# Optimization experiments

Measured on AMD Instinct MI355X. Metric: run time of the kernel, lower is better.

## Reference

```python
import jax, jax.numpy as jnp
import numpy as np


def setup_inputs() -> dict:
    key = jax.random.key(0)
    k1, k2, k3 = jax.random.split(key, 3)
    B, L, D = 32, 8192, 512
    q = jax.random.normal(k1, (B, D), dtype=jnp.float32)
    k = jax.random.normal(k2, (B, L, D), dtype=jnp.float32)
    v = jax.random.normal(k3, (B, L, D), dtype=jnp.float32)
    return {"q": q, "k": k, "v": v}


def reference(q, k, v):
    # q: [B, D], k: [B, L, D], v: [B, L, D]
    # scores: [B, 1, L]  (single query per batch element, no 1/sqrt(d) scaling
    # in the original module)
    scores = jnp.einsum("bd,bld->bl", q, k)[:, None, :]
    # double softmax over the key dimension, exactly as the torch module
    att_weights = jax.nn.softmax(scores, axis=-1)
    att_score = jax.nn.softmax(att_weights, axis=-1)
    # ctx: [B, D]
    ctx = jnp.einsum("bsl,bld->bsd", att_score, v)[:, 0, :]
    return (ctx, att_score)
```

## Files before the change

kernel.cpp:

```cpp
#include <hip/hip_runtime.h>
#include <hip/hip_bf16.h>
#include <stdint.h>

#define B_ 32
#define L_ 8192
#define D_ 512

__global__ __launch_bounds__(256) void k_scores(const float* __restrict__ q,
                                                const float* __restrict__ k,
                                                float* __restrict__ scores) {
    int blk  = blockIdx.x;
    int b    = blk >> 7;
    int l0   = (blk & 127) << 6;
    int wave = threadIdx.x >> 6;
    int lane = threadIdx.x & 63;

    float4 q0 = *reinterpret_cast<const float4*>(q + b * D_ + lane * 4);
    float4 q1 = *reinterpret_cast<const float4*>(q + b * D_ + 256 + lane * 4);

    const size_t kbase = (size_t)b * L_ * D_;
    for (int i = 0; i < 16; i++) {
        int l = l0 + i * 4 + wave;
        const float* kr = k + kbase + (size_t)l * D_;
        float4 a0 = *reinterpret_cast<const float4*>(kr + lane * 4);
        float4 a1 = *reinterpret_cast<const float4*>(kr + 256 + lane * 4);
        float s = a0.x * q0.x + a0.y * q0.y + a0.z * q0.z + a0.w * q0.w
                + a1.x * q1.x + a1.y * q1.y + a1.z * q1.z + a1.w * q1.w;
        #pragma unroll
        for (int off = 32; off; off >>= 1) s += __shfl_xor(s, off, 64);
        if (lane == 0) scores[b * L_ + l] = s;
    }
}

__global__ __launch_bounds__(1024) void k_softmax2(float* __restrict__ sc,
                                                   float* __restrict__ att_out) {
    int b = blockIdx.x;
    int t = threadIdx.x;
    int wid = t >> 6, lane = t & 63;
    __shared__ float red[16];

    float s[8];
    #pragma unroll
    for (int j = 0; j < 8; j++) s[j] = sc[b * L_ + t + j * 1024];

    float m = s[0];
    #pragma unroll
    for (int j = 1; j < 8; j++) m = fmaxf(m, s[j]);
    #pragma unroll
    for (int off = 32; off; off >>= 1) m = fmaxf(m, __shfl_xor(m, off, 64));
    if (lane == 0) red[wid] = m;
    __syncthreads();
    m = red[0];
    #pragma unroll
    for (int i = 1; i < 16; i++) m = fmaxf(m, red[i]);
    __syncthreads();

    float e[8]; float sum = 0.f;
    #pragma unroll
    for (int j = 0; j < 8; j++) { e[j] = expf(s[j] - m); sum += e[j]; }
    #pragma unroll
    for (int off = 32; off; off >>= 1) sum += __shfl_xor(sum, off, 64);
    if (lane == 0) red[wid] = sum;
    __syncthreads();
    float Z = 0.f;
    #pragma unroll
    for (int i = 0; i < 16; i++) Z += red[i];
    __syncthreads();

    float invZ = 1.f / Z;
    float maxw = invZ;

    float p[8]; float sum2 = 0.f;
    #pragma unroll
    for (int j = 0; j < 8; j++) { p[j] = expf(e[j] * invZ - maxw); sum2 += p[j]; }
    #pragma unroll
    for (int off = 32; off; off >>= 1) sum2 += __shfl_xor(sum2, off, 64);
    if (lane == 0) red[wid] = sum2;
    __syncthreads();
    float S2 = 0.f;
    #pragma unroll
    for (int i = 0; i < 16; i++) S2 += red[i];

    float invS2 = 1.f / S2;
    #pragma unroll
    for (int j = 0; j < 8; j++) {
        float a = p[j] * invS2;
        int idx = b * L_ + t + j * 1024;
        sc[idx] = a;
        att_out[idx] = a;
    }
}

__global__ __launch_bounds__(256) void k_ctx_partial(const float* __restrict__ v,
                                                     const float* __restrict__ att,
                                                     float* __restrict__ part) {
    int blk  = blockIdx.x;
    int b    = blk >> 5;
    int c    = blk & 31;
    int t    = threadIdx.x;
    int half = t >> 7;
    int dt   = (t & 127) * 4;

    float acc[4] = {0.f, 0.f, 0.f, 0.f};
    const size_t vbase = (size_t)b * L_ * D_;
    int lbase = c * 256 + half;
    for (int i = 0; i < 128; i++) {
        int l = lbase + i * 2;
        float a = att[b * L_ + l];
        float4 vv = *reinterpret_cast<const float4*>(v + vbase + (size_t)l * D_ + dt);
        acc[0] += a * vv.x; acc[1] += a * vv.y;
        acc[2] += a * vv.z; acc[3] += a * vv.w;
    }
    float* dst = part + ((size_t)(b * 64 + c * 2 + half)) * D_ + dt;
    dst[0] = acc[0]; dst[1] = acc[1]; dst[2] = acc[2]; dst[3] = acc[3];
}

__global__ __launch_bounds__(512) void k_ctx_reduce(const float* __restrict__ part,
                                                    float* __restrict__ ctx) {
    int b = blockIdx.x;
    int d = threadIdx.x;
    float s = 0.f;
    for (int r = 0; r < 64; r++) s += part[((size_t)(b * 64 + r)) * D_ + d];
    ctx[b * D_ + d] = s;
}

extern "C" void kernel_launch(void* const* d_in, const int* in_sizes, int n_in,
                              void* d_out, int out_size, void* d_ws, size_t ws_size,
                              hipStream_t stream) {
    const float* q = (const float*)d_in[0];
    const float* k = (const float*)d_in[1];
    const float* v = (const float*)d_in[2];
    float* out     = (float*)d_out;
    float* ctx_out = out;
    float* att_out = out + B_ * D_;

    float* scores = (float*)d_ws;
    float* part   = scores + B_ * L_;

    k_scores     <<<B_ * (L_ / 64), 256, 0, stream>>>(q, k, scores);
    k_softmax2   <<<B_,             1024, 0, stream>>>(scores, att_out);
    k_ctx_partial<<<B_ * 32,        256,  0, stream>>>(v, scores, part);
    k_ctx_reduce <<<B_,             512,  0, stream>>>(part, ctx_out);
}
```

Measured before the change: 207.6 us.

## Fuse ctx reduction into partial kernel via atomics and drop duplicate score write

Removes the separate ctx reduction kernel. Each ctx-partial block now combines its two halves in shared memory and atomically adds the sum into ctx, which the softmax kernel zeroes first. The softmax no longer writes the attention weights back to the scores buffer; the ctx kernel reads them from the output instead. Unroll pragmas are added to the score and ctx loops. This saves a launch, a partials round trip and one write, but adds float atomics whose summation order is nondeterministic.

Result: faster. 201.9 us (-2.8%).

```diff
diff --git a/kernel.cpp b/kernel.cpp
--- a/kernel.cpp
+++ b/kernel.cpp
@@ -19,6 +19,7 @@
     float4 q1 = *reinterpret_cast<const float4*>(q + b * D_ + 256 + lane * 4);
 
     const size_t kbase = (size_t)b * L_ * D_;
+    #pragma unroll 4
     for (int i = 0; i < 16; i++) {
         int l = l0 + i * 4 + wave;
         const float* kr = k + kbase + (size_t)l * D_;
@@ -32,12 +33,15 @@
     }
 }
 
-__global__ __launch_bounds__(1024) void k_softmax2(float* __restrict__ sc,
-                                                   float* __restrict__ att_out) {
+__global__ __launch_bounds__(1024) void k_softmax2(const float* __restrict__ sc,
+                                                   float* __restrict__ att_out,
+                                                   float* __restrict__ ctx) {
     int b = blockIdx.x;
     int t = threadIdx.x;
     int wid = t >> 6, lane = t & 63;
     __shared__ float red[16];
+
+    if (t < D_) ctx[b * D_ + t] = 0.f;
 
     float s[8];
     #pragma unroll
@@ -84,26 +88,25 @@
     float invS2 = 1.f / S2;
     #pragma unroll
     for (int j = 0; j < 8; j++) {
-        float a = p[j] * invS2;
-        int idx = b * L_ + t + j * 1024;
-        sc[idx] = a;
-        att_out[idx] = a;
+        att_out[b * L_ + t + j * 1024] = p[j] * invS2;
     }
 }
 
 __global__ __launch_bounds__(256) void k_ctx_partial(const float* __restrict__ v,
                                                      const float* __restrict__ att,
-                                                     float* __restrict__ part) {
+                                                     float* __restrict__ ctx) {
     int blk  = blockIdx.x;
     int b    = blk >> 5;
     int c    = blk & 31;
     int t    = threadIdx.x;
     int half = t >> 7;
     int dt   = (t & 127) * 4;
+    __shared__ float4 red4[128];
 
     float acc[4] = {0.f, 0.f, 0.f, 0.f};
     const size_t vbase = (size_t)b * L_ * D_;
     int lbase = c * 256 + half;
+    #pragma unroll 8
     for (int i = 0; i < 128; i++) {
         int l = lbase + i * 2;
         float a = att[b * L_ + l];
@@ -111,17 +114,16 @@
         acc[0] += a * vv.x; acc[1] += a * vv.y;
         acc[2] += a * vv.z; acc[3] += a * vv.w;
     }
-    float* dst = part + ((size_t)(b * 64 + c * 2 + half)) * D_ + dt;
-    dst[0] = acc[0]; dst[1] = acc[1]; dst[2] = acc[2]; dst[3] = acc[3];
-}
-
-__global__ __launch_bounds__(512) void k_ctx_reduce(const float* __restrict__ part,
-                                                    float* __restrict__ ctx) {
-    int b = blockIdx.x;
-    int d = threadIdx.x;
-    float s = 0.f;
-    for (int r = 0; r < 64; r++) s += part[((size_t)(b * 64 + r)) * D_ + d];
-    ctx[b * D_ + d] = s;
+    if (half) red4[t & 127] = make_float4(acc[0], acc[1], acc[2], acc[3]);
+    __syncthreads();
+    if (!half) {
+        float4 r = red4[t];
+        float* dst = ctx + b * D_ + dt;
+        atomicAdd(dst + 0, acc[0] + r.x);
+        atomicAdd(dst + 1, acc[1] + r.y);
+        atomicAdd(dst + 2, acc[2] + r.z);
+        atomicAdd(dst + 3, acc[3] + r.w);
+    }
 }
 
 extern "C" void kernel_launch(void* const* d_in, const int* in_sizes, int n_in,
@@ -135,10 +137,8 @@
     float* att_out = out + B_ * D_;
 
     float* scores = (float*)d_ws;
-    float* part   = scores + B_ * L_;
 
-    k_scores     <<<B_ * (L_ / 64), 256, 0, stream>>>(q, k, scores);
-    k_softmax2   <<<B_,             1024, 0, stream>>>(scores, att_out);
-    k_ctx_partial<<<B_ * 32,        256,  0, stream>>>(v, scores, part);
-    k_ctx_reduce <<<B_,             512,  0, stream>>>(part, ctx_out);
+    k_scores     <<<B_ * (L_ / 64), 256,  0, stream>>>(q, k, scores);
+    k_softmax2   <<<B_,             1024, 0, stream>>>(scores, att_out, ctx_out);
+    k_ctx_partial<<<B_ * 32,        256,  0, stream>>>(v, att_out, ctx_out);
 }
```
